# Kernel optimization log

Hardware: AMD Instinct MI355X
Metric: run time of the kernel (lower is better)

Reference implementation:

```python
import math
import jax, jax.numpy as jnp
import numpy as np

BATCH, L, H, M, K = 16, 4096, 256, 256, 4

def setup_inputs() -> dict:
    key = jax.random.key(0)
    ks = jax.random.split(key, 12)
    inputs = jax.random.normal(ks[0], (BATCH, L, H), jnp.float32)
    b_std = 1.0 / math.sqrt(H)
    c_std = 1.0 / math.sqrt(M)
    B_param = jax.random.uniform(ks[1], (M, H, 2), jnp.float32, -b_std, b_std)
    C_param = jax.random.uniform(ks[2], (H, M, 2), jnp.float32, -c_std, c_std)
    D = jax.random.normal(ks[3], (H,), jnp.float32)
    enc_w = jax.random.normal(ks[4], (H, H), jnp.float32) * (1.0 / math.sqrt(H))
    enc_b = jnp.zeros((H,), jnp.float32)
    conv_w = jax.random.normal(ks[5], (H, 1, K), jnp.float32) * (1.0 / math.sqrt(K))
    conv_b = jnp.zeros((H,), jnp.float32)
    # ring init: r in [0.9,1.0], theta in (0,pi)
    r0 = jnp.sqrt(jax.random.uniform(ks[6], (M,), jnp.float32) * (1.0 - 0.81) + 0.81)
    r0 = jnp.clip(r0, 0.9, 0.999)
    th0 = jax.random.uniform(ks[7], (M,), jnp.float32, 0.05, math.pi - 0.05)
    r_logit_base = jnp.log(r0 / (1.0 - r0))
    th_atanh_base = jnp.arctanh(th0 / math.pi)
    # heads are zero-init in the module; use small random so the selective path is exercised
    r_head_w = jax.random.normal(ks[8], (M, H), jnp.float32) * 0.01
    th_head_w = jax.random.normal(ks[9], (M, H), jnp.float32) * 0.01
    dt_base = jax.random.normal(ks[10], (M,), jnp.float32) * 0.5
    inj_head_w = jax.random.normal(ks[11], (M, H), jnp.float32) * 0.01
    return {"inputs": inputs, "B_param": B_param, "C_param": C_param, "D": D,
            "enc_w": enc_w, "enc_b": enc_b, "conv_w": conv_w, "conv_b": conv_b,
            "r_logit_base": r_logit_base, "th_atanh_base": th_atanh_base,
            "r_head_w": r_head_w, "th_head_w": th_head_w, "dt_base": dt_base,
            "inj_head_w": inj_head_w}

def _forward(inputs, B_param, C_param, D, enc_w, enc_b, conv_w, conv_b,
             r_logit_base, th_atanh_base, r_head_w, th_head_w, dt_base, inj_head_w):
    silu = jax.nn.silu
    # encoder: linear -> SiLU -> depthwise causal conv (left pad K-1) -> SiLU
    feats = silu(inputs @ enc_w.T + enc_b)                      # (B,L,H)
    fc = jnp.transpose(feats, (0, 2, 1))                        # (B,H,L)
    conv = jax.lax.conv_general_dilated(
        fc, conv_w, window_strides=(1,), padding=[(K - 1, 0)],
        dimension_numbers=("NCH", "OIH", "NCH"), feature_group_count=H)
    feats = silu(jnp.transpose(conv + conv_b[None, :, None], (0, 2, 1)))  # (B,L,H)
    # spectral conditioning
    r = jax.nn.sigmoid(r_logit_base + feats @ r_head_w.T)       # (B,L,M)
    theta = math.pi * jnp.tanh(th_atanh_base + feats @ th_head_w.T)
    dt = jax.nn.sigmoid(dt_base)                                # (M,) per_step_dt=False
    dtc = jnp.maximum(dt, 1e-6)
    r2 = jnp.maximum(r * r, 1e-8)
    A = jnp.maximum((r2 - 2.0 * r * jnp.cos(theta) + 1.0) / (dtc * dtc * r2), 0.0)
    G = jnp.maximum((1.0 - r2) / (dtc * r2), 0.0)
    # complex input projection + selective injection gate
    bu = jax.lax.complex(inputs @ B_param[..., 0].T, inputs @ B_param[..., 1].T)  # (B,L,M) c64
    gate = jax.nn.sigmoid(feats @ inj_head_w.T)
    bu = bu * gate
    # time-major for scan
    A_s = jnp.transpose(A, (1, 0, 2))
    G_s = jnp.transpose(G, (1, 0, 2))
    bu_s = jnp.transpose(bu, (1, 0, 2))
    z0 = jnp.zeros((inputs.shape[0], M), jnp.complex64)
    x0 = jnp.zeros((inputs.shape[0], M), jnp.complex64)

    def step(carry, t_in):  # imex1 variant
        z, x = carry
        A_t, G_t, bu_t = t_in
        S = 1.0 + dtc * G_t
        z = (z + dtc * (-A_t * x + bu_t)) / jnp.maximum(S, 1e-6)
        x = x + dtc * z
        return (z, x), x

    _, xs = jax.lax.scan(step, (z0, x0), (A_s, G_s, bu_s))      # (L,B,M) complex64
    proj = (jnp.einsum("lbm,hm->lbh", xs.real, C_param[..., 0])
            - jnp.einsum("lbm,hm->lbh", xs.imag, C_param[..., 1]))
    proj = jnp.transpose(proj, (1, 0, 2))                       # (B,L,H)
    return proj + D * inputs

def reference(inputs, B_param, C_param, D, enc_w, enc_b, conv_w, conv_b,
              r_logit_base, th_atanh_base, r_head_w, th_head_w, dt_base, inj_head_w):
    return _forward(inputs, B_param, C_param, D, enc_w, enc_b, conv_w, conv_b,
                    r_logit_base, th_atanh_base, r_head_w, th_head_w, dt_base, inj_head_w)
```

## Files before the change

### kernel.cpp

```cpp
#include <hip/hip_runtime.h>

#define H_ 256
#define M_ 256
#define L_ 4096
#define B_ 16
#define PI_F 3.14159265358979323846f

typedef unsigned short u16;
typedef __attribute__((ext_vector_type(8))) short short8v;
typedef __attribute__((ext_vector_type(4))) float floatx4;

__device__ __forceinline__ float sigm(float x) { return 1.0f / (1.0f + expf(-x)); }
__device__ __forceinline__ u16 f2bf(float f) {
    unsigned int u = __float_as_uint(f);
    unsigned int r = (u + 0x7fff + ((u >> 16) & 1)) >> 16;
    return (u16)r;
}
__device__ __forceinline__ float bf2f(u16 h) { return __uint_as_float(((unsigned int)h) << 16); }
__device__ __forceinline__ void split2(float x, u16& h, u16& l) {
    h = f2bf(x);
    l = f2bf(x - bf2f(h));
}

__global__ __launch_bounds__(256) void k_prep(const float* __restrict__ Bp,
                                              const float* __restrict__ Cp,
                                              const float* __restrict__ enc_w,
                                              const float* __restrict__ Wr,
                                              const float* __restrict__ Wt,
                                              const float* __restrict__ Wg,
                                              const float* __restrict__ dtb,
                                              u16* __restrict__ EWhi, u16* __restrict__ EWlo,
                                              u16* __restrict__ HWhi, u16* __restrict__ HWlo,
                                              u16* __restrict__ GWhi,
                                              u16* __restrict__ WBh,
                                              u16* __restrict__ Chath,
                                              float* __restrict__ dtc, float* __restrict__ idt,
                                              float* __restrict__ idt2) {
    int tid = blockIdx.x * 256 + threadIdx.x;
    if (tid < M_) {
        float d = fmaxf(sigm(dtb[tid]), 1e-6f);
        dtc[tid] = d;
        idt[tid] = 1.0f / d;
        idt2[tid] = 1.0f / (d * d);
    }
    u16 h, l;
    split2(enc_w[tid], h, l); EWhi[tid] = h; EWlo[tid] = l;
    split2(Wr[tid], h, l);    HWhi[tid] = h; HWlo[tid] = l;
    split2(Wt[tid], h, l);    HWhi[65536 + tid] = h; HWlo[65536 + tid] = l;
    GWhi[tid] = f2bf(Wg[tid]);
    WBh[tid]         = f2bf(Bp[2 * tid + 0]);
    WBh[65536 + tid] = f2bf(Bp[2 * tid + 1]);
    int hh = tid >> 8, m = tid & (M_ - 1);
    Chath[hh * 512 + 2 * m + 0] = f2bf(Cp[2 * tid + 0]);
    Chath[hh * 512 + 2 * m + 1] = f2bf(-Cp[2 * tid + 1]);
}

__global__ __launch_bounds__(256) void k_zero(float* __restrict__ p, int n) {
    int i = blockIdx.x * 256 + threadIdx.x;
    if (i < n) p[i] = 0.0f;
}

template <int NH, int NPROD, int EPI, bool AGLOB>
__global__ __launch_bounds__(256) void k_sgemm(const float* __restrict__ A,
                                               const u16* __restrict__ Whi,
                                               const u16* __restrict__ Wlo,
                                               void* __restrict__ OUTv,
                                               const u16* __restrict__ g16,
                                               const float* __restrict__ p0,
                                               const float* __restrict__ p1,
                                               const float* __restrict__ p2,
                                               const float* __restrict__ p3,
                                               int K, int C, int t0) {
    constexpr int LOR = (NPROD == 3) ? 128 : 1;
    constexpr int NBL = (NPROD == 3) ? NH : 1;
    __shared__ u16 Ah[128][40];
    __shared__ u16 Al[LOR][40];
    __shared__ u16 Bh[NH][128][40];
    __shared__ u16 Bl[NBL][LOR][40];
    const int tid = threadIdx.x;
    const int tpb = C >> 7;
    const int batch = blockIdx.y / tpb;
    const int i0 = (blockIdx.y % tpb) << 7;
    const int colBase = blockIdx.x << 7;
    const int aRow0 = AGLOB ? (batch * L_ + t0 + i0) : (batch * C + i0);
    const int oRow0 = batch * C + i0;
    const int arow = tid >> 1, aseg = (tid & 1) << 4;
    const float* pa = &A[(size_t)(aRow0 + arow) * K + aseg];
    float4 ra0 = *(const float4*)pa, ra1 = *(const float4*)(pa + 4);
    float4 ra2 = *(const float4*)(pa + 8), ra3 = *(const float4*)(pa + 12);
    const int lane = tid & 63, wv = tid >> 6;
    const int wr = wv >> 1, wc = wv & 1;
    const int fr = lane & 15, kg = lane >> 4;
    floatx4 acc[NH][4][4];
#pragma unroll
    for (int h = 0; h < NH; ++h)
#pragma unroll
        for (int i = 0; i < 4; ++i)
#pragma unroll
            for (int j = 0; j < 4; ++j) acc[h][i][j] = (floatx4){0.f, 0.f, 0.f, 0.f};
    const int KT = K >> 5;
    for (int kt = 0; kt < KT; ++kt) {
        short8v rbh[NH][2], rbl[NBL][2];
#pragma unroll
        for (int h = 0; h < NH; ++h) {
            const u16* pb = &Whi[(size_t)h * 65536 + (size_t)(colBase + arow) * K + kt * 32 + aseg];
            rbh[h][0] = *(const short8v*)pb; rbh[h][1] = *(const short8v*)(pb + 8);
            if (NPROD == 3) {
                const u16* pl = &Wlo[(size_t)h * 65536 + (size_t)(colBase + arow) * K + kt * 32 + aseg];
                rbl[h][0] = *(const short8v*)pl; rbl[h][1] = *(const short8v*)(pl + 8);
            }
        }
        __syncthreads();
        {
            u16 hb[16], lb[16];
            float v[16] = {ra0.x, ra0.y, ra0.z, ra0.w, ra1.x, ra1.y, ra1.z, ra1.w,
                           ra2.x, ra2.y, ra2.z, ra2.w, ra3.x, ra3.y, ra3.z, ra3.w};
#pragma unroll
            for (int s = 0; s < 16; ++s) {
                if (NPROD == 3) split2(v[s], hb[s], lb[s]);
                else hb[s] = f2bf(v[s]);
            }
            *(short8v*)&Ah[arow][aseg] = *(short8v*)&hb[0];
            *(short8v*)&Ah[arow][aseg + 8] = *(short8v*)&hb[8];
            if (NPROD == 3) {
                *(short8v*)&Al[arow][aseg] = *(short8v*)&lb[0];
                *(short8v*)&Al[arow][aseg + 8] = *(short8v*)&lb[8];
            }
        }
#pragma unroll
        for (int h = 0; h < NH; ++h) {
            *(short8v*)&Bh[h][arow][aseg] = rbh[h][0];
            *(short8v*)&Bh[h][arow][aseg + 8] = rbh[h][1];
            if (NPROD == 3) {
                *(short8v*)&Bl[h][arow][aseg] = rbl[h][0];
                *(short8v*)&Bl[h][arow][aseg + 8] = rbl[h][1];
            }
        }
        __syncthreads();
        if (kt + 1 < KT) {
            pa += 32;
            ra0 = *(const float4*)pa; ra1 = *(const float4*)(pa + 4);
            ra2 = *(const float4*)(pa + 8); ra3 = *(const float4*)(pa + 12);
        }
        short8v afh[4], afl[4];
#pragma unroll
        for (int i = 0; i < 4; ++i) afh[i] = *(short8v*)&Ah[wr * 64 + i * 16 + fr][kg << 3];
        if (NPROD == 3) {
#pragma unroll
            for (int i = 0; i < 4; ++i) afl[i] = *(short8v*)&Al[wr * 64 + i * 16 + fr][kg << 3];
        }
#pragma unroll
        for (int h = 0; h < NH; ++h) {
            short8v bfh[4], bfl[4];
#pragma unroll
            for (int j = 0; j < 4; ++j) bfh[j] = *(short8v*)&Bh[h][wc * 64 + j * 16 + fr][kg << 3];
            if (NPROD == 3) {
#pragma unroll
                for (int j = 0; j < 4; ++j) bfl[j] = *(short8v*)&Bl[h][wc * 64 + j * 16 + fr][kg << 3];
            }
#pragma unroll
            for (int i = 0; i < 4; ++i)
#pragma unroll
                for (int j = 0; j < 4; ++j) {
                    floatx4 t = acc[h][i][j];
                    if (NPROD == 3) {
                        t = __builtin_amdgcn_mfma_f32_16x16x32_bf16(afl[i], bfh[j], t, 0, 0, 0);
                        t = __builtin_amdgcn_mfma_f32_16x16x32_bf16(afh[i], bfl[j], t, 0, 0, 0);
                    }
                    t = __builtin_amdgcn_mfma_f32_16x16x32_bf16(afh[i], bfh[j], t, 0, 0, 0);
                    acc[h][i][j] = t;
                }
        }
    }
#pragma unroll
    for (int i = 0; i < 4; ++i)
#pragma unroll
        for (int j = 0; j < 4; ++j) {
            int rbase = wr * 64 + i * 16 + (kg << 2);
            int col = colBase + wc * 64 + j * 16 + fr;
#pragma unroll
            for (int r = 0; r < 4; ++r) {
                int orow = oRow0 + rbase + r;
                if (EPI == 1) {
                    float v = acc[0][i][j][r] + p0[col];
                    ((float*)OUTv)[(size_t)orow * 256 + col] = v * sigm(v);
                } else if (EPI == 2) {
                    ((u16*)OUTv)[(size_t)orow * 256 + col] = f2bf(sigm(acc[0][i][j][r]));
                } else if (EPI == 0) {
                    float rr = sigm(p0[col] + acc[0][i][j][r]);
                    float th = PI_F * tanhf(p1[col] + acc[1][i][j][r]);
                    float r2 = fmaxf(rr * rr, 1e-8f);
                    float Av = fmaxf((r2 - 2.0f * rr * cosf(th) + 1.0f) * p3[col] / r2, 0.0f);
                    float Gv = fmaxf((1.0f - r2) * p2[col] / r2, 0.0f);
                    *(float2*)&((float*)OUTv)[((size_t)orow * 256 + col) * 2] = make_float2(Av, Gv);
                } else {
                    float g = bf2f(g16[(size_t)orow * 256 + col]);
#pragma unroll
                    for (int h = 0; h < NH; ++h)
                        ((u16*)OUTv)[(size_t)orow * 512 + h * 256 + col] = f2bf(acc[h][i][j][r] * g);
                }
            }
        }
}

__global__ __launch_bounds__(256) void k_conv(const float* __restrict__ F0,
                                              const float* __restrict__ TAIL,
                                              const float* __restrict__ cw,
                                              const float* __restrict__ cb,
                                              float* __restrict__ F,
                                              int t0, int C) {
    int idx = blockIdx.x * 256 + threadIdx.x;
    int h = idx & (H_ - 1);
    int rl = idx >> 8;
    int b = rl / C;
    int dtl = rl - b * C;
    int t = t0 + dtl;
    float w0 = cw[h * 4 + 0], w1 = cw[h * 4 + 1], w2 = cw[h * 4 + 2], w3 = cw[h * 4 + 3];
    float acc = cb[h];
    acc = fmaf(F0[(size_t)rl * H_ + h], w3, acc);
#pragma unroll
    for (int kk = 1; kk <= 3; ++kk) {
        float w = (kk == 1) ? w2 : (kk == 2) ? w1 : w0;
        if (t - kk >= 0) {
            float src;
            if (dtl - kk >= 0) src = F0[(size_t)(rl - kk) * H_ + h];
            else               src = TAIL[((b * 3 + (3 + dtl - kk)) << 8) + h];
            acc = fmaf(src, w, acc);
        }
    }
    F[(size_t)rl * H_ + h] = acc * sigm(acc);
}

__global__ __launch_bounds__(256) void k_tail(const float* __restrict__ F0,
                                              float* __restrict__ TAIL, int C) {
    int b = blockIdx.x / 3, j = blockIdx.x % 3, h = threadIdx.x;
    TAIL[((b * 3 + j) << 8) + h] = F0[((size_t)(b * C + C - 3 + j) << 8) + h];
}

#define SEG_ 64
__global__ __launch_bounds__(256) void k_scan1(const float* __restrict__ AGf2,
                                               const u16* __restrict__ BUh,
                                               const float* __restrict__ dtc_,
                                               float* __restrict__ SEGM,
                                               float* __restrict__ SEGV,
                                               int C) {
    int m = threadIdx.x;
    int nseg = C >> 6;
    int b = blockIdx.x / nseg;
    int s = blockIdx.x - b * nseg;
    float dt = dtc_[m];
    size_t row0 = (size_t)b * C + s * SEG_;
    float a = 1.f, bb = 0.f, c = 0.f, d = 1.f;
    float vzr = 0.f, vzi = 0.f, vxr = 0.f, vxi = 0.f;
    for (int t = 0; t < SEG_; ++t) {
        size_t row = row0 + t;
        float2 ag = *(const float2*)&AGf2[(row * 256 + m) * 2];
        float br = bf2f(BUh[row * 512 + m]);
        float bi = bf2f(BUh[row * 512 + 256 + m]);
        float S = fmaf(dt, ag.y, 1.0f);
        float e = 1.0f / fmaxf(S, 1e-6f);
        float sa = e;
        float sb = -dt * ag.x * e;
        float sc = dt * e;
        float sd = fmaf(dt, sb, 1.0f);
        float na = fmaf(sa, a, sb * c), nb = fmaf(sa, bb, sb * d);
        float nc = fmaf(sc, a, sd * c), nd = fmaf(sc, bb, sd * d);
        float wz = dt * e;
        float nvzr = fmaf(sa, vzr, fmaf(sb, vxr, wz * br));
        float nvzi = fmaf(sa, vzi, fmaf(sb, vxi, wz * bi));
        float nvxr = fmaf(sc, vzr, fmaf(sd, vxr, dt * wz * br));
        float nvxi = fmaf(sc, vzi, fmaf(sd, vxi, dt * wz * bi));
        a = na; bb = nb; c = nc; d = nd;
        vzr = nvzr; vzi = nvzi; vxr = nvxr; vxi = nvxi;
    }
    size_t o = ((size_t)blockIdx.x * M_ + m) * 4;
    *(float4*)&SEGM[o] = make_float4(a, bb, c, d);
    *(float4*)&SEGV[o] = make_float4(vzr, vzi, vxr, vxi);
}

__global__ __launch_bounds__(256) void k_scan2(const float* __restrict__ SEGM,
                                               const float* __restrict__ SEGV,
                                               float* __restrict__ carry,
                                               float* __restrict__ PRE,
                                               int C) {
    int m = threadIdx.x;
    int b = blockIdx.x;
    int nseg = C >> 6;
    float4 st = *(float4*)&carry[(size_t)(b * M_ + m) * 4];
    for (int s = 0; s < nseg; ++s) {
        size_t o = ((size_t)(b * nseg + s) * M_ + m) * 4;
        *(float4*)&PRE[o] = st;
        float4 Mm = *(const float4*)&SEGM[o];
        float4 Vv = *(const float4*)&SEGV[o];
        float nzr = fmaf(Mm.x, st.x, fmaf(Mm.y, st.z, Vv.x));
        float nzi = fmaf(Mm.x, st.y, fmaf(Mm.y, st.w, Vv.y));
        float nxr = fmaf(Mm.z, st.x, fmaf(Mm.w, st.z, Vv.z));
        float nxi = fmaf(Mm.z, st.y, fmaf(Mm.w, st.w, Vv.w));
        st = make_float4(nzr, nzi, nxr, nxi);
    }
    *(float4*)&carry[(size_t)(b * M_ + m) * 4] = st;
}

__global__ __launch_bounds__(256) void k_scan3p(const float* __restrict__ AGf2,
                                                const u16* __restrict__ BUh,
                                                const float* __restrict__ dtc_,
                                                const float* __restrict__ PRE,
                                                const u16* __restrict__ Chath,
                                                const float* __restrict__ Dv,
                                                const float* __restrict__ X0,
                                                float* __restrict__ OUT,
                                                int t0, int C) {
    __shared__ u16 XT[32][520];
    __shared__ u16 Bs[256][40];
    const int tid = threadIdx.x;
    const int m = tid;
    const int nseg = C >> 6;
    const int b = blockIdx.x / nseg;
    const int s = blockIdx.x - b * nseg;
    const float dt = dtc_[m];
    float4 st = *(const float4*)&PRE[((size_t)blockIdx.x * M_ + m) * 4];
    float zr = st.x, zi = st.y, xr = st.z, xi = st.w;
    const size_t row0 = (size_t)b * C + s * SEG_;
    const int grow0 = b * L_ + t0 + s * SEG_;
    const int lane = tid & 63, wc = tid >> 6;
    const int fr = lane & 15, kg = lane >> 4;
#pragma unroll
    for (int half = 0; half < 2; ++half) {
        for (int t = 0; t < 32; ++t) {
            size_t row = row0 + half * 32 + t;
            float2 ag = *(const float2*)&AGf2[(row * 256 + m) * 2];
            float br = bf2f(BUh[row * 512 + m]);
            float bi = bf2f(BUh[row * 512 + 256 + m]);
            float S = fmaf(dt, ag.y, 1.0f);
            float inv = 1.0f / fmaxf(S, 1e-6f);
            zr = fmaf(dt, fmaf(-ag.x, xr, br), zr) * inv;
            zi = fmaf(dt, fmaf(-ag.x, xi, bi), zi) * inv;
            xr = fmaf(dt, zr, xr);
            xi = fmaf(dt, zi, xi);
            unsigned int pk = (unsigned int)f2bf(xr) | ((unsigned int)f2bf(xi) << 16);
            *(unsigned int*)&XT[t][2 * m] = pk;
        }
        __syncthreads();
        floatx4 pacc[2][4];
#pragma unroll
        for (int i = 0; i < 2; ++i)
#pragma unroll
            for (int j = 0; j < 4; ++j) pacc[i][j] = (floatx4){0.f, 0.f, 0.f, 0.f};
        for (int kc = 0; kc < 16; ++kc) {
            const u16* pc = &Chath[(size_t)tid * 512 + kc * 32];
            short8v c0 = *(const short8v*)pc;
            short8v c1 = *(const short8v*)(pc + 8);
            short8v c2 = *(const short8v*)(pc + 16);
            short8v c3 = *(const short8v*)(pc + 24);
            *(short8v*)&Bs[tid][0]  = c0;
            *(short8v*)&Bs[tid][8]  = c1;
            *(short8v*)&Bs[tid][16] = c2;
            *(short8v*)&Bs[tid][24] = c3;
            __syncthreads();
            short8v af[2], bf[4];
#pragma unroll
            for (int i = 0; i < 2; ++i) af[i] = *(short8v*)&XT[i * 16 + fr][kc * 32 + (kg << 3)];
#pragma unroll
            for (int j = 0; j < 4; ++j) bf[j] = *(short8v*)&Bs[wc * 64 + j * 16 + fr][kg << 3];
#pragma unroll
            for (int i = 0; i < 2; ++i)
#pragma unroll
                for (int j = 0; j < 4; ++j)
                    pacc[i][j] = __builtin_amdgcn_mfma_f32_16x16x32_bf16(af[i], bf[j], pacc[i][j], 0, 0, 0);
            __syncthreads();
        }
#pragma unroll
        for (int i = 0; i < 2; ++i)
#pragma unroll
            for (int j = 0; j < 4; ++j) {
                int col = wc * 64 + j * 16 + fr;
#pragma unroll
                for (int r = 0; r < 4; ++r) {
                    int grow = grow0 + half * 32 + i * 16 + (kg << 2) + r;
                    OUT[(size_t)grow * 256 + col] =
                        fmaf(Dv[col], X0[(size_t)grow * 256 + col], pacc[i][j][r]);
                }
            }
        __syncthreads();
    }
}

extern "C" void kernel_launch(void* const* d_in, const int* in_sizes, int n_in,
                              void* d_out, int out_size, void* d_ws, size_t ws_size,
                              hipStream_t stream) {
    const float* inputs = (const float*)d_in[0];
    const float* Bp     = (const float*)d_in[1];
    const float* Cp     = (const float*)d_in[2];
    const float* Dv     = (const float*)d_in[3];
    const float* enc_w  = (const float*)d_in[4];
    const float* enc_b  = (const float*)d_in[5];
    const float* conv_w = (const float*)d_in[6];
    const float* conv_b = (const float*)d_in[7];
    const float* rlb    = (const float*)d_in[8];
    const float* tab    = (const float*)d_in[9];
    const float* Wr     = (const float*)d_in[10];
    const float* Wt     = (const float*)d_in[11];
    const float* dtb    = (const float*)d_in[12];
    const float* Wg     = (const float*)d_in[13];

    int C = 4096;
    while (C > 128) {
        size_t need = (size_t)B_ * C * 5632 + (48ull << 20);
        if (need <= ws_size) break;
        C >>= 1;
    }

    char* ws = (char*)d_ws;
    size_t off = 0;
    auto alloc = [&](size_t bytes) -> char* {
        char* p = ws + off;
        off = (off + bytes + 1023) & ~(size_t)1023;
        return p;
    };
    const int rows = B_ * C;
    const int nseg = C >> 6;
    float* F0   = (float*)alloc((size_t)rows * 256 * 4);
    float* F    = (float*)alloc((size_t)rows * 256 * 4);
    float* AGf2 = (float*)alloc((size_t)rows * 512 * 4);
    u16*   GTh  = (u16*)alloc((size_t)rows * 256 * 2);
    u16*   BUh  = (u16*)alloc((size_t)rows * 512 * 2);
    float* SEGM = (float*)alloc((size_t)B_ * nseg * M_ * 16);
    float* SEGV = (float*)alloc((size_t)B_ * nseg * M_ * 16);
    float* PRE  = (float*)alloc((size_t)B_ * nseg * M_ * 16);
    u16* EWhi = (u16*)alloc(65536 * 2);
    u16* EWlo = (u16*)alloc(65536 * 2);
    u16* HWhi = (u16*)alloc(2 * 65536 * 2);
    u16* HWlo = (u16*)alloc(2 * 65536 * 2);
    u16* GWhi = (u16*)alloc(65536 * 2);
    u16* WBh  = (u16*)alloc(2 * 65536 * 2);
    u16* Chath= (u16*)alloc(2 * 65536 * 2);
    float* dtc  = (float*)alloc(1024);
    float* idt  = (float*)alloc(1024);
    float* idt2 = (float*)alloc(1024);
    float* carry= (float*)alloc(B_ * M_ * 16);
    float* TAIL = (float*)alloc(B_ * 3 * 256 * 4);

    const int NC = L_ / C;
    const int tpb = C >> 7;

    k_prep<<<256, 256, 0, stream>>>(Bp, Cp, enc_w, Wr, Wt, Wg, dtb,
                                    EWhi, EWlo, HWhi, HWlo, GWhi, WBh, Chath, dtc, idt, idt2);
    k_zero<<<(B_ * M_ * 4 + 255) / 256, 256, 0, stream>>>(carry, B_ * M_ * 4);

    for (int c = 0; c < NC; ++c) {
        int t0 = c * C;
        k_sgemm<1, 3, 1, true><<<dim3(2, B_ * tpb), 256, 0, stream>>>(
            inputs, EWhi, EWlo, F0, nullptr, enc_b, nullptr, nullptr, nullptr, 256, C, t0);
        k_conv<<<rows, 256, 0, stream>>>(F0, TAIL, conv_w, conv_b, F, t0, C);
        k_tail<<<B_ * 3, 256, 0, stream>>>(F0, TAIL, C);
        k_sgemm<2, 3, 0, false><<<dim3(2, B_ * tpb), 256, 0, stream>>>(
            F, HWhi, HWlo, AGf2, nullptr, rlb, tab, idt, idt2, 256, C, t0);
        k_sgemm<1, 1, 2, false><<<dim3(2, B_ * tpb), 256, 0, stream>>>(
            F, GWhi, nullptr, GTh, nullptr, nullptr, nullptr, nullptr, nullptr, 256, C, t0);
        k_sgemm<2, 1, 3, true><<<dim3(2, B_ * tpb), 256, 0, stream>>>(
            inputs, WBh, nullptr, BUh, GTh, nullptr, nullptr, nullptr, nullptr, 256, C, t0);
        k_scan1<<<B_ * nseg, 256, 0, stream>>>(AGf2, BUh, dtc, SEGM, SEGV, C);
        k_scan2<<<B_, 256, 0, stream>>>(SEGM, SEGV, carry, PRE, C);
        k_scan3p<<<B_ * nseg, 256, 0, stream>>>(AGf2, BUh, dtc, PRE, Chath, Dv, inputs,
                                                (float*)d_out, t0, C);
    }
}
```

Baseline: 725.1 us.

## Fuse GEMMs sharing an A operand and pre-split conv output into bf16 hi/lo

The four per-chunk GEMM launches become two. One handles the encoder plus the B projection, since both read the raw inputs. The other handles the r/theta heads plus the gate, since all three read the conv features. The conv kernel now writes its output already split into bf16 hi/lo, so the second GEMM no longer re-splits fp32 activations for every tile. The gate multiply on the B projection moves into the scan kernels, which now read GTh and scale br/bi on the fly. The cost is more accumulator registers per fused GEMM (NH=3), which may lower occupancy, plus an extra gate read inside both scan passes.

New measurement: 844.5 us. 1.16x slower.

```diff
diff --git a/kernel.cpp b/kernel.cpp
--- a/kernel.cpp
+++ b/kernel.cpp
@@ -29,10 +29,8 @@
                                               const float* __restrict__ Wt,
                                               const float* __restrict__ Wg,
                                               const float* __restrict__ dtb,
-                                              u16* __restrict__ EWhi, u16* __restrict__ EWlo,
-                                              u16* __restrict__ HWhi, u16* __restrict__ HWlo,
-                                              u16* __restrict__ GWhi,
-                                              u16* __restrict__ WBh,
+                                              u16* __restrict__ W1h, u16* __restrict__ W1l,
+                                              u16* __restrict__ W2h, u16* __restrict__ W2l,
                                               u16* __restrict__ Chath,
                                               float* __restrict__ dtc, float* __restrict__ idt,
                                               float* __restrict__ idt2) {
@@ -44,12 +42,12 @@
         idt2[tid] = 1.0f / (d * d);
     }
     u16 h, l;
-    split2(enc_w[tid], h, l); EWhi[tid] = h; EWlo[tid] = l;
-    split2(Wr[tid], h, l);    HWhi[tid] = h; HWlo[tid] = l;
-    split2(Wt[tid], h, l);    HWhi[65536 + tid] = h; HWlo[65536 + tid] = l;
-    GWhi[tid] = f2bf(Wg[tid]);
-    WBh[tid]         = f2bf(Bp[2 * tid + 0]);
-    WBh[65536 + tid] = f2bf(Bp[2 * tid + 1]);
+    split2(enc_w[tid], h, l); W1h[tid] = h; W1l[tid] = l;
+    W1h[65536 + tid]  = f2bf(Bp[2 * tid + 0]);
+    W1h[131072 + tid] = f2bf(Bp[2 * tid + 1]);
+    split2(Wr[tid], h, l); W2h[tid] = h; W2l[tid] = l;
+    split2(Wt[tid], h, l); W2h[65536 + tid] = h; W2l[65536 + tid] = l;
+    W2h[131072 + tid] = f2bf(Wg[tid]);
     int hh = tid >> 8, m = tid & (M_ - 1);
     Chath[hh * 512 + 2 * m + 0] = f2bf(Cp[2 * tid + 0]);
     Chath[hh * 512 + 2 * m + 1] = f2bf(-Cp[2 * tid + 1]);
@@ -60,23 +58,23 @@
     if (i < n) p[i] = 0.0f;
 }
 
-template <int NH, int NPROD, int EPI, bool AGLOB>
-__global__ __launch_bounds__(256) void k_sgemm(const float* __restrict__ A,
+template <int NH, int NSPLIT, int EPI, bool AGLOB, bool APRE>
+__global__ __launch_bounds__(256) void k_fgemm(const float* __restrict__ Af,
+                                               const u16* __restrict__ Ahi,
+                                               const u16* __restrict__ Alo,
                                                const u16* __restrict__ Whi,
                                                const u16* __restrict__ Wlo,
-                                               void* __restrict__ OUTv,
-                                               const u16* __restrict__ g16,
+                                               float* __restrict__ OUT1,
+                                               u16* __restrict__ OUT2,
                                                const float* __restrict__ p0,
                                                const float* __restrict__ p1,
                                                const float* __restrict__ p2,
                                                const float* __restrict__ p3,
                                                int K, int C, int t0) {
-    constexpr int LOR = (NPROD == 3) ? 128 : 1;
-    constexpr int NBL = (NPROD == 3) ? NH : 1;
     __shared__ u16 Ah[128][40];
-    __shared__ u16 Al[LOR][40];
+    __shared__ u16 Al[128][40];
     __shared__ u16 Bh[NH][128][40];
-    __shared__ u16 Bl[NBL][LOR][40];
+    __shared__ u16 Bl[NSPLIT][128][40];
     const int tid = threadIdx.x;
     const int tpb = C >> 7;
     const int batch = blockIdx.y / tpb;
@@ -85,9 +83,20 @@
     const int aRow0 = AGLOB ? (batch * L_ + t0 + i0) : (batch * C + i0);
     const int oRow0 = batch * C + i0;
     const int arow = tid >> 1, aseg = (tid & 1) << 4;
-    const float* pa = &A[(size_t)(aRow0 + arow) * K + aseg];
-    float4 ra0 = *(const float4*)pa, ra1 = *(const float4*)(pa + 4);
-    float4 ra2 = *(const float4*)(pa + 8), ra3 = *(const float4*)(pa + 12);
+    float4 ra0, ra1, ra2, ra3;
+    short8v rah0, rah1, ral0, ral1;
+    const float* paf = nullptr;
+    const u16 *pah = nullptr, *pal = nullptr;
+    if constexpr (APRE) {
+        pah = &Ahi[(size_t)(aRow0 + arow) * K + aseg];
+        pal = &Alo[(size_t)(aRow0 + arow) * K + aseg];
+        rah0 = *(const short8v*)pah; rah1 = *(const short8v*)(pah + 8);
+        ral0 = *(const short8v*)pal; ral1 = *(const short8v*)(pal + 8);
+    } else {
+        paf = &Af[(size_t)(aRow0 + arow) * K + aseg];
+        ra0 = *(const float4*)paf;       ra1 = *(const float4*)(paf + 4);
+        ra2 = *(const float4*)(paf + 8); ra3 = *(const float4*)(paf + 12);
+    }
     const int lane = tid & 63, wv = tid >> 6;
     const int wr = wv >> 1, wc = wv & 1;
     const int fr = lane & 15, kg = lane >> 4;
@@ -100,61 +109,65 @@
             for (int j = 0; j < 4; ++j) acc[h][i][j] = (floatx4){0.f, 0.f, 0.f, 0.f};
     const int KT = K >> 5;
     for (int kt = 0; kt < KT; ++kt) {
-        short8v rbh[NH][2], rbl[NBL][2];
+        short8v rbh[NH][2], rbl[NSPLIT > 0 ? NSPLIT : 1][2];
 #pragma unroll
         for (int h = 0; h < NH; ++h) {
             const u16* pb = &Whi[(size_t)h * 65536 + (size_t)(colBase + arow) * K + kt * 32 + aseg];
             rbh[h][0] = *(const short8v*)pb; rbh[h][1] = *(const short8v*)(pb + 8);
-            if (NPROD == 3) {
-                const u16* pl = &Wlo[(size_t)h * 65536 + (size_t)(colBase + arow) * K + kt * 32 + aseg];
-                rbl[h][0] = *(const short8v*)pl; rbl[h][1] = *(const short8v*)(pl + 8);
-            }
+        }
+#pragma unroll
+        for (int h = 0; h < NSPLIT; ++h) {
+            const u16* pl = &Wlo[(size_t)h * 65536 + (size_t)(colBase + arow) * K + kt * 32 + aseg];
+            rbl[h][0] = *(const short8v*)pl; rbl[h][1] = *(const short8v*)(pl + 8);
         }
         __syncthreads();
-        {
+        if constexpr (APRE) {
+            *(short8v*)&Ah[arow][aseg] = rah0; *(short8v*)&Ah[arow][aseg + 8] = rah1;
+            *(short8v*)&Al[arow][aseg] = ral0; *(short8v*)&Al[arow][aseg + 8] = ral1;
+        } else {
             u16 hb[16], lb[16];
             float v[16] = {ra0.x, ra0.y, ra0.z, ra0.w, ra1.x, ra1.y, ra1.z, ra1.w,
                            ra2.x, ra2.y, ra2.z, ra2.w, ra3.x, ra3.y, ra3.z, ra3.w};
 #pragma unroll
-            for (int s = 0; s < 16; ++s) {
-                if (NPROD == 3) split2(v[s], hb[s], lb[s]);
-                else hb[s] = f2bf(v[s]);
-            }
+            for (int s = 0; s < 16; ++s) split2(v[s], hb[s], lb[s]);
             *(short8v*)&Ah[arow][aseg] = *(short8v*)&hb[0];
             *(short8v*)&Ah[arow][aseg + 8] = *(short8v*)&hb[8];
-            if (NPROD == 3) {
-                *(short8v*)&Al[arow][aseg] = *(short8v*)&lb[0];
-                *(short8v*)&Al[arow][aseg + 8] = *(short8v*)&lb[8];
-            }
+            *(short8v*)&Al[arow][aseg] = *(short8v*)&lb[0];
+            *(short8v*)&Al[arow][aseg + 8] = *(short8v*)&lb[8];
         }
 #pragma unroll
         for (int h = 0; h < NH; ++h) {
             *(short8v*)&Bh[h][arow][aseg] = rbh[h][0];
             *(short8v*)&Bh[h][arow][aseg + 8] = rbh[h][1];
-            if (NPROD == 3) {
-                *(short8v*)&Bl[h][arow][aseg] = rbl[h][0];
-                *(short8v*)&Bl[h][arow][aseg + 8] = rbl[h][1];
-            }
+        }
+#pragma unroll
+        for (int h = 0; h < NSPLIT; ++h) {
+            *(short8v*)&Bl[h][arow][aseg] = rbl[h][0];
+            *(short8v*)&Bl[h][arow][aseg + 8] = rbl[h][1];
         }
         __syncthreads();
         if (kt + 1 < KT) {
-            pa += 32;
-            ra0 = *(const float4*)pa; ra1 = *(const float4*)(pa + 4);
-            ra2 = *(const float4*)(pa + 8); ra3 = *(const float4*)(pa + 12);
+            if constexpr (APRE) {
+                pah += 32; pal += 32;
+                rah0 = *(const short8v*)pah; rah1 = *(const short8v*)(pah + 8);
+                ral0 = *(const short8v*)pal; ral1 = *(const short8v*)(pal + 8);
+            } else {
+                paf += 32;
+                ra0 = *(const float4*)paf;       ra1 = *(const float4*)(paf + 4);
+                ra2 = *(const float4*)(paf + 8); ra3 = *(const float4*)(paf + 12);
+            }
         }
         short8v afh[4], afl[4];
 #pragma unroll
         for (int i = 0; i < 4; ++i) afh[i] = *(short8v*)&Ah[wr * 64 + i * 16 + fr][kg << 3];
-        if (NPROD == 3) {
-#pragma unroll
-            for (int i = 0; i < 4; ++i) afl[i] = *(short8v*)&Al[wr * 64 + i * 16 + fr][kg << 3];
-        }
+#pragma unroll
+        for (int i = 0; i < 4; ++i) afl[i] = *(short8v*)&Al[wr * 64 + i * 16 + fr][kg << 3];
 #pragma unroll
         for (int h = 0; h < NH; ++h) {
             short8v bfh[4], bfl[4];
 #pragma unroll
             for (int j = 0; j < 4; ++j) bfh[j] = *(short8v*)&Bh[h][wc * 64 + j * 16 + fr][kg << 3];
-            if (NPROD == 3) {
+            if (h < NSPLIT) {
 #pragma unroll
                 for (int j = 0; j < 4; ++j) bfl[j] = *(short8v*)&Bl[h][wc * 64 + j * 16 + fr][kg << 3];
             }
@@ -163,7 +176,7 @@
 #pragma unroll
                 for (int j = 0; j < 4; ++j) {
                     floatx4 t = acc[h][i][j];
-                    if (NPROD == 3) {
+                    if (h < NSPLIT) {
                         t = __builtin_amdgcn_mfma_f32_16x16x32_bf16(afl[i], bfh[j], t, 0, 0, 0);
                         t = __builtin_amdgcn_mfma_f32_16x16x32_bf16(afh[i], bfl[j], t, 0, 0, 0);
                     }
@@ -181,23 +194,19 @@
 #pragma unroll
             for (int r = 0; r < 4; ++r) {
                 int orow = oRow0 + rbase + r;
-                if (EPI == 1) {
+                if constexpr (EPI == 1) {
                     float v = acc[0][i][j][r] + p0[col];
-                    ((float*)OUTv)[(size_t)orow * 256 + col] = v * sigm(v);
-                } else if (EPI == 2) {
-                    ((u16*)OUTv)[(size_t)orow * 256 + col] = f2bf(sigm(acc[0][i][j][r]));
-                } else if (EPI == 0) {
+                    OUT1[(size_t)orow * 256 + col] = v * sigm(v);
+                    OUT2[(size_t)orow * 512 + col] = f2bf(acc[1][i][j][r]);
+                    OUT2[(size_t)orow * 512 + 256 + col] = f2bf(acc[2][i][j][r]);
+                } else {
                     float rr = sigm(p0[col] + acc[0][i][j][r]);
                     float th = PI_F * tanhf(p1[col] + acc[1][i][j][r]);
                     float r2 = fmaxf(rr * rr, 1e-8f);
                     float Av = fmaxf((r2 - 2.0f * rr * cosf(th) + 1.0f) * p3[col] / r2, 0.0f);
                     float Gv = fmaxf((1.0f - r2) * p2[col] / r2, 0.0f);
-                    *(float2*)&((float*)OUTv)[((size_t)orow * 256 + col) * 2] = make_float2(Av, Gv);
-                } else {
-                    float g = bf2f(g16[(size_t)orow * 256 + col]);
-#pragma unroll
-                    for (int h = 0; h < NH; ++h)
-                        ((u16*)OUTv)[(size_t)orow * 512 + h * 256 + col] = f2bf(acc[h][i][j][r] * g);
+                    *(float2*)&OUT1[((size_t)orow * 256 + col) * 2] = make_float2(Av, Gv);
+                    OUT2[(size_t)orow * 256 + col] = f2bf(sigm(acc[2][i][j][r]));
                 }
             }
         }
@@ -207,7 +216,8 @@
                                               const float* __restrict__ TAIL,
                                               const float* __restrict__ cw,
                                               const float* __restrict__ cb,
-                                              float* __restrict__ F,
+                                              u16* __restrict__ Fhi,
+                                              u16* __restrict__ Flo,
                                               int t0, int C) {
     int idx = blockIdx.x * 256 + threadIdx.x;
     int h = idx & (H_ - 1);
@@ -228,7 +238,11 @@
             acc = fmaf(src, w, acc);
         }
     }
-    F[(size_t)rl * H_ + h] = acc * sigm(acc);
+    float y = acc * sigm(acc);
+    u16 hh, ll;
+    split2(y, hh, ll);
+    Fhi[(size_t)rl * H_ + h] = hh;
+    Flo[(size_t)rl * H_ + h] = ll;
 }
 
 __global__ __launch_bounds__(256) void k_tail(const float* __restrict__ F0,
@@ -240,6 +254,7 @@
 #define SEG_ 64
 __global__ __launch_bounds__(256) void k_scan1(const float* __restrict__ AGf2,
                                                const u16* __restrict__ BUh,
+                                               const u16* __restrict__ GTh,
                                                const float* __restrict__ dtc_,
                                                float* __restrict__ SEGM,
                                                float* __restrict__ SEGV,
@@ -255,8 +270,9 @@
     for (int t = 0; t < SEG_; ++t) {
         size_t row = row0 + t;
         float2 ag = *(const float2*)&AGf2[(row * 256 + m) * 2];
-        float br = bf2f(BUh[row * 512 + m]);
-        float bi = bf2f(BUh[row * 512 + 256 + m]);
+        float g = bf2f(GTh[row * 256 + m]);
+        float br = bf2f(BUh[row * 512 + m]) * g;
+        float bi = bf2f(BUh[row * 512 + 256 + m]) * g;
         float S = fmaf(dt, ag.y, 1.0f);
         float e = 1.0f / fmaxf(S, 1e-6f);
         float sa = e;
@@ -303,6 +319,7 @@
 
 __global__ __launch_bounds__(256) void k_scan3p(const float* __restrict__ AGf2,
                                                 const u16* __restrict__ BUh,
+                                                const u16* __restrict__ GTh,
                                                 const float* __restrict__ dtc_,
                                                 const float* __restrict__ PRE,
                                                 const u16* __restrict__ Chath,
@@ -329,8 +346,9 @@
         for (int t = 0; t < 32; ++t) {
             size_t row = row0 + half * 32 + t;
             float2 ag = *(const float2*)&AGf2[(row * 256 + m) * 2];
-            float br = bf2f(BUh[row * 512 + m]);
-            float bi = bf2f(BUh[row * 512 + 256 + m]);
+            float g = bf2f(GTh[row * 256 + m]);
+            float br = bf2f(BUh[row * 512 + m]) * g;
+            float bi = bf2f(BUh[row * 512 + 256 + m]) * g;
             float S = fmaf(dt, ag.y, 1.0f);
             float inv = 1.0f / fmaxf(S, 1e-6f);
             zr = fmaf(dt, fmaf(-ag.x, xr, br), zr) * inv;
@@ -420,19 +438,18 @@
     const int rows = B_ * C;
     const int nseg = C >> 6;
     float* F0   = (float*)alloc((size_t)rows * 256 * 4);
-    float* F    = (float*)alloc((size_t)rows * 256 * 4);
+    u16*   Fhi  = (u16*)alloc((size_t)rows * 256 * 2);
+    u16*   Flo  = (u16*)alloc((size_t)rows * 256 * 2);
     float* AGf2 = (float*)alloc((size_t)rows * 512 * 4);
     u16*   GTh  = (u16*)alloc((size_t)rows * 256 * 2);
     u16*   BUh  = (u16*)alloc((size_t)rows * 512 * 2);
     float* SEGM = (float*)alloc((size_t)B_ * nseg * M_ * 16);
     float* SEGV = (float*)alloc((size_t)B_ * nseg * M_ * 16);
     float* PRE  = (float*)alloc((size_t)B_ * nseg * M_ * 16);
-    u16* EWhi = (u16*)alloc(65536 * 2);
-    u16* EWlo = (u16*)alloc(65536 * 2);
-    u16* HWhi = (u16*)alloc(2 * 65536 * 2);
-    u16* HWlo = (u16*)alloc(2 * 65536 * 2);
-    u16* GWhi = (u16*)alloc(65536 * 2);
-    u16* WBh  = (u16*)alloc(2 * 65536 * 2);
+    u16* W1h  = (u16*)alloc(3 * 65536 * 2);
+    u16* W1l  = (u16*)alloc(1 * 65536 * 2);
+    u16* W2h  = (u16*)alloc(3 * 65536 * 2);
+    u16* W2l  = (u16*)alloc(2 * 65536 * 2);
     u16* Chath= (u16*)alloc(2 * 65536 * 2);
     float* dtc  = (float*)alloc(1024);
     float* idt  = (float*)alloc(1024);
@@ -444,24 +461,22 @@
     const int tpb = C >> 7;
 
     k_prep<<<256, 256, 0, stream>>>(Bp, Cp, enc_w, Wr, Wt, Wg, dtb,
-                                    EWhi, EWlo, HWhi, HWlo, GWhi, WBh, Chath, dtc, idt, idt2);
+                                    W1h, W1l, W2h, W2l, Chath, dtc, idt, idt2);
     k_zero<<<(B_ * M_ * 4 + 255) / 256, 256, 0, stream>>>(carry, B_ * M_ * 4);
 
     for (int c = 0; c < NC; ++c) {
         int t0 = c * C;
-        k_sgemm<1, 3, 1, true><<<dim3(2, B_ * tpb), 256, 0, stream>>>(
-            inputs, EWhi, EWlo, F0, nullptr, enc_b, nullptr, nullptr, nullptr, 256, C, t0);
-        k_conv<<<rows, 256, 0, stream>>>(F0, TAIL, conv_w, conv_b, F, t0, C);
+        k_fgemm<3, 1, 1, true, false><<<dim3(2, B_ * tpb), 256, 0, stream>>>(
+            inputs, nullptr, nullptr, W1h, W1l, F0, BUh,
+            enc_b, nullptr, nullptr, nullptr, 256, C, t0);
+        k_conv<<<rows, 256, 0, stream>>>(F0, TAIL, conv_w, conv_b, Fhi, Flo, t0, C);
         k_tail<<<B_ * 3, 256, 0, stream>>>(F0, TAIL, C);
-        k_sgemm<2, 3, 0, false><<<dim3(2, B_ * tpb), 256, 0, stream>>>(
-            F, HWhi, HWlo, AGf2, nullptr, rlb, tab, idt, idt2, 256, C, t0);
-        k_sgemm<1, 1, 2, false><<<dim3(2, B_ * tpb), 256, 0, stream>>>(
-            F, GWhi, nullptr, GTh, nullptr, nullptr, nullptr, nullptr, nullptr, 256, C, t0);
-        k_sgemm<2, 1, 3, true><<<dim3(2, B_ * tpb), 256, 0, stream>>>(
-            inputs, WBh, nullptr, BUh, GTh, nullptr, nullptr, nullptr, nullptr, 256, C, t0);
-        k_scan1<<<B_ * nseg, 256, 0, stream>>>(AGf2, BUh, dtc, SEGM, SEGV, C);
+        k_fgemm<3, 2, 0, false, true><<<dim3(2, B_ * tpb), 256, 0, stream>>>(
+            nullptr, Fhi, Flo, W2h, W2l, AGf2, GTh,
+            rlb, tab, idt, idt2, 256, C, t0);
+        k_scan1<<<B_ * nseg, 256, 0, stream>>>(AGf2, BUh, GTh, dtc, SEGM, SEGV, C);
         k_scan2<<<B_, 256, 0, stream>>>(SEGM, SEGV, carry, PRE, C);
-        k_scan3p<<<B_ * nseg, 256, 0, stream>>>(AGf2, BUh, dtc, PRE, Chath, Dv, inputs,
+        k_scan3p<<<B_ * nseg, 256, 0, stream>>>(AGf2, BUh, GTh, dtc, PRE, Chath, Dv, inputs,
                                                 (float*)d_out, t0, C);
     }
 }
```
